# Optimization experiments

Hardware: AMD Instinct MI355X
Metric: run time of the kernel (lower is better)

## Reference

```python
import jax, jax.numpy as jnp
import numpy as np

B, T, C = 1, 2048, 2048
N_HEAD, N_KV = 32, 8
HD = C // N_HEAD            # 64
N_REP = N_HEAD // N_KV      # 4
WINDOW = 512                # sliding_window
N_GLOBAL = 16               # n_global_tokens


def setup_inputs() -> dict:
    key = jax.random.key(0)
    ks = jax.random.split(key, 5)
    x = jax.random.normal(ks[0], (B, T, C), jnp.float32)
    # standard RoPE frequency tables, shape (T, HD//2)
    inv_freq = 1.0 / (10000.0 ** (np.arange(0, HD, 2, dtype=np.float32) / HD))
    ang = np.outer(np.arange(T, dtype=np.float32), inv_freq)
    freqs_cos = jnp.asarray(np.cos(ang), jnp.float32)
    freqs_sin = jnp.asarray(np.sin(ang), jnp.float32)
    s = 0.02
    wq = jax.random.normal(ks[1], (C, C), jnp.float32) * s
    wk = jax.random.normal(ks[2], (N_KV * HD, C), jnp.float32) * s
    wv = jax.random.normal(ks[3], (N_KV * HD, C), jnp.float32) * s
    wo = jax.random.normal(ks[4], (C, C), jnp.float32) * s
    return {"x": x, "freqs_cos": freqs_cos, "freqs_sin": freqs_sin,
            "wq": wq, "wk": wk, "wv": wv, "wo": wo}


def _apply_rope(xh, fc, fs):
    # xh: (B, H, T, HD); fc/fs: (T, HD//2) broadcast over (B, H)
    xr = xh.reshape(*xh.shape[:-1], HD // 2, 2)
    x0, x1 = xr[..., 0], xr[..., 1]
    fc = fc[None, None]
    fs = fs[None, None]
    out = jnp.stack([x0 * fc - x1 * fs, x0 * fs + x1 * fc], axis=-1)
    return out.reshape(xh.shape)


def reference(x, freqs_cos, freqs_sin, wq, wk, wv, wo):
    Bx, Tx, Cx = x.shape
    q = (x @ wq.T).reshape(Bx, Tx, N_HEAD, HD).transpose(0, 2, 1, 3)   # (B,Hq,T,hd)
    k = (x @ wk.T).reshape(Bx, Tx, N_KV, HD).transpose(0, 2, 1, 3)     # (B,Hkv,T,hd)
    v = (x @ wv.T).reshape(Bx, Tx, N_KV, HD).transpose(0, 2, 1, 3)
    q = _apply_rope(q, freqs_cos, freqs_sin)
    k = _apply_rope(k, freqs_cos, freqs_sin)

    # GQA: group query heads over shared kv heads instead of repeat_kv
    qg = q.reshape(Bx, N_KV, N_REP, Tx, HD)
    scale = 1.0 / float(np.sqrt(HD))
    scores = jnp.einsum('bgrqd,bgkd->bgrqk', qg, k) * scale  # (B,G,R,T,T)

    # sliding-window causal mask with global tokens (kv_cache=None branch)
    q_pos = jnp.arange(Tx)[:, None]
    k_pos = jnp.arange(Tx)[None, :]
    mask = (k_pos <= q_pos) & (k_pos >= q_pos - (WINDOW - 1))
    mask = mask | (k_pos < N_GLOBAL)
    # note: global columns combined with causal rows always leave >=1 valid key
    scores = jnp.where(mask[None, None, None], scores, -jnp.inf)
    probs = jax.nn.softmax(scores, axis=-1)

    y = jnp.einsum('bgrqk,bgkd->bgrqd', probs, v)
    y = y.reshape(Bx, N_HEAD, Tx, HD).transpose(0, 2, 1, 3).reshape(Bx, Tx, Cx)
    return y @ wo.T  # dropout p=0 in eval
```

## Files before the change

kernel.cpp:

```cpp
#include <hip/hip_runtime.h>
#include <hip/hip_bf16.h>

using short8 = __attribute__((ext_vector_type(8))) short;
using f32x4  = __attribute__((ext_vector_type(4))) float;
using f32x16 = __attribute__((ext_vector_type(16))) float;
using int4v  = __attribute__((ext_vector_type(4))) int;

#define T_SEQ  2048
#define C_DIM  2048
#define NH     32
#define NKV    8
#define HD     64
#define WINDOW 512
#define NGLOB  16

__device__ inline ushort f2bf(float f) {
  union { float f; unsigned u; } v; v.f = f;
  unsigned u = v.u;
  u += 0x7fffu + ((u >> 16) & 1u);
  return (ushort)(u >> 16);
}
__device__ inline float bf2f(ushort h) {
  union { unsigned u; float f; } v; v.u = ((unsigned)h) << 16;
  return v.f;
}

__device__ __forceinline__ void gl_lds16(const ushort* g, ushort* l) {
  __builtin_amdgcn_global_load_lds(
      (const __attribute__((address_space(1))) void*)g,
      (__attribute__((address_space(3))) void*)l, 16, 0, 0);
}

__device__ __forceinline__ f32x16 zero16() {
  f32x16 v;
#pragma unroll
  for (int i = 0; i < 16; i++) v[i] = 0.f;
  return v;
}

__global__ void cvt_f32_bf16(const float* __restrict__ in, ushort* __restrict__ out, int n8) {
  int i = blockIdx.x * blockDim.x + threadIdx.x;
  int stride = gridDim.x * blockDim.x;
  for (; i < n8; i += stride) {
    f32x4 a = *reinterpret_cast<const f32x4*>(in + (size_t)i * 8);
    f32x4 b = *reinterpret_cast<const f32x4*>(in + (size_t)i * 8 + 4);
    short8 o;
#pragma unroll
    for (int j = 0; j < 4; j++) { o[j] = (short)f2bf(a[j]); o[4 + j] = (short)f2bf(b[j]); }
    *reinterpret_cast<short8*>(out + (size_t)i * 8) = o;
  }
}

template <int MODE>
__global__ __launch_bounds__(512) void gemm2p(const ushort* __restrict__ A,
                                              const ushort* __restrict__ B0,
                                              const ushort* __restrict__ B1,
                                              const ushort* __restrict__ B2,
                                              void* __restrict__ C0,
                                              void* __restrict__ C1,
                                              void* __restrict__ C2,
                                              int K) {
  __shared__ ushort As[2][2][128][32];
  __shared__ ushort Bs[2][2][128][32];
  const int tid  = threadIdx.x;
  const int lane = tid & 63;
  const int wid  = tid >> 6;
  const int wr = wid >> 2, wc = wid & 3;
  const int r16 = lane & 15, g16 = (lane >> 4) & 3;
  const int bx = blockIdx.x, by = blockIdx.y;

  const ushort* Brow;
  void* Cout;
  int ldc, col0;
  if constexpr (MODE == 1) {
    if (bx < 16)      { Brow = B0 + (size_t)bx * 128 * K;        Cout = C0; ldc = 2048; col0 = bx * 128; }
    else if (bx < 20) { Brow = B1 + (size_t)(bx - 16) * 128 * K; Cout = C1; ldc = 512;  col0 = (bx - 16) * 128; }
    else              { Brow = B2 + (size_t)(bx - 20) * 128 * K; Cout = C2; ldc = 512;  col0 = (bx - 20) * 128; }
  } else {
    Brow = B0 + (size_t)bx * 128 * K; Cout = C0; ldc = 2048; col0 = bx * 128;
  }
  const ushort* Arow = A + (size_t)by * 128 * K;

  f32x4 acc[4][2];
#pragma unroll
  for (int i = 0; i < 4; i++)
#pragma unroll
    for (int j = 0; j < 2; j++) acc[i][j] = (f32x4){0.f, 0.f, 0.f, 0.f};

  const int srow = tid >> 2, scch = tid & 3;
  const int ssc  = scch ^ ((srow >> 1) & 3);
  const size_t agoff = (size_t)srow * K + ssc * 8;
  const int rchunk = (g16 ^ ((r16 >> 1) & 3)) * 8;

  const int nt = K >> 6;
  int d = 0;

#define STAGE(dd, k0)                                                         \
  {                                                                           \
    _Pragma("unroll") for (int kk = 0; kk < 2; kk++) {                        \
      gl_lds16(&Arow[agoff + (k0) + kk * 32], &As[dd][kk][srow][scch * 8]);   \
      gl_lds16(&Brow[agoff + (k0) + kk * 32], &Bs[dd][kk][srow][scch * 8]);   \
    }                                                                         \
  }

  STAGE(0, 0);
  __syncthreads();

  for (int t = 0; t < nt; ++t) {
    if (t + 1 < nt) STAGE(d ^ 1, (t + 1) * 64);
#pragma unroll
    for (int kk = 0; kk < 2; kk++) {
      short8 af[4], bfv[2];
#pragma unroll
      for (int i = 0; i < 4; i++)
        af[i] = *reinterpret_cast<const short8*>(&As[d][kk][wr * 64 + i * 16 + r16][rchunk]);
#pragma unroll
      for (int j = 0; j < 2; j++)
        bfv[j] = *reinterpret_cast<const short8*>(&Bs[d][kk][wc * 32 + j * 16 + r16][rchunk]);
#pragma unroll
      for (int i = 0; i < 4; i++)
#pragma unroll
        for (int j = 0; j < 2; j++)
          acc[i][j] = __builtin_amdgcn_mfma_f32_16x16x32_bf16(af[i], bfv[j], acc[i][j], 0, 0, 0);
    }
    __syncthreads();
    d ^= 1;
  }
#undef STAGE

#pragma unroll
  for (int i = 0; i < 4; i++)
#pragma unroll
    for (int j = 0; j < 2; j++) {
      int col = col0 + wc * 32 + j * 16 + r16;
#pragma unroll
      for (int r = 0; r < 4; r++) {
        int row = by * 128 + wr * 64 + i * 16 + g16 * 4 + r;
        if constexpr (MODE == 0) ((float*)Cout)[(size_t)row * ldc + col] = acc[i][j][r];
        else                     ((ushort*)Cout)[(size_t)row * ldc + col] = f2bf(acc[i][j][r]);
      }
    }
}

__global__ void rope2(ushort* __restrict__ Qb, ushort* __restrict__ Kb,
                      const float* __restrict__ fc, const float* __restrict__ fs) {
  int idx = blockIdx.x * blockDim.x + threadIdx.x;
  const int QN = T_SEQ * NH * 8;
  ushort* X; int t, hh, c, ld;
  if (idx < QN) { X = Qb; c = idx & 7; hh = (idx >> 3) & 31; t = idx >> 8; ld = NH * HD; }
  else { idx -= QN; X = Kb; c = idx & 7; hh = (idx >> 3) & 7; t = idx >> 6; ld = NKV * HD; }
  size_t base = (size_t)t * ld + hh * HD + c * 8;
  short8 v = *reinterpret_cast<const short8*>(&X[base]);
  f32x4 cc = *reinterpret_cast<const f32x4*>(&fc[t * 32 + c * 4]);
  f32x4 ss = *reinterpret_cast<const f32x4*>(&fs[t * 32 + c * 4]);
  short8 o;
#pragma unroll
  for (int j = 0; j < 4; j++) {
    float x0 = bf2f((ushort)v[2 * j]), x1 = bf2f((ushort)v[2 * j + 1]);
    o[2 * j]     = (short)f2bf(x0 * cc[j] - x1 * ss[j]);
    o[2 * j + 1] = (short)f2bf(x0 * ss[j] + x1 * cc[j]);
  }
  *reinterpret_cast<short8*>(&X[base]) = o;
}

__global__ __launch_bounds__(256) void transpose_bf16(const ushort* __restrict__ in,
                                                      ushort* __restrict__ out,
                                                      int R, int Cc) {
  __shared__ ushort tile[64][72];
  int tr = blockIdx.y * 64, tc = blockIdx.x * 64;
  int tid = threadIdx.x;
#pragma unroll
  for (int s = 0; s < 2; s++) {
    int idx = tid + s * 256;
    int row = idx >> 3, c8 = idx & 7;
    short8 v = *reinterpret_cast<const short8*>(&in[(size_t)(tr + row) * Cc + tc + c8 * 8]);
#pragma unroll
    for (int j = 0; j < 8; j++) tile[row][c8 * 8 + j] = (ushort)v[j];
  }
  __syncthreads();
#pragma unroll
  for (int s = 0; s < 2; s++) {
    int idx = tid + s * 256;
    int orow = idx >> 3, c8 = idx & 7;
    short8 v;
#pragma unroll
    for (int j = 0; j < 8; j++) v[j] = (short)tile[c8 * 8 + j][orow];
    *reinterpret_cast<short8*>(&out[(size_t)(tc + orow) * R + tr + c8 * 8]) = v;
  }
}

__global__ __launch_bounds__(256) void attn32(const ushort* __restrict__ Q,
                                              const ushort* __restrict__ K,
                                              const ushort* __restrict__ Vt,
                                              ushort* __restrict__ Y) {
  __shared__ ushort Ot[4][32][72];
  const int lane = threadIdx.x & 63;
  const int wv   = threadIdx.x >> 6;
  const int h  = blockIdx.x >> 4;
  const int qt = ((blockIdx.x & 15) << 2) + wv;
  const int q0 = qt << 5;
  const int g  = h >> 2;
  const int l31 = lane & 31, hi = lane >> 5;
  const int hi8 = hi << 3, hi4 = hi << 2;
  const int qrow = q0 + l31;
  const float KLOG = 0.125f * 1.44269504089f;

  short8 qf[4];
#pragma unroll
  for (int s = 0; s < 4; s++)
    qf[s] = *reinterpret_cast<const short8*>(&Q[(size_t)qrow * C_DIM + h * HD + s * 16 + hi8]);

  f32x16 o[2] = { zero16(), zero16() };
  float mrow = -1e30f, ssum = 0.f;

  auto pack8 = [&](const float* pp) -> short8 {
    unsigned wA, wB, wC, wD;
    asm("v_cvt_pk_bf16_f32 %0, %1, %2" : "=v"(wA) : "v"(pp[0]), "v"(pp[1]));
    asm("v_cvt_pk_bf16_f32 %0, %1, %2" : "=v"(wB) : "v"(pp[2]), "v"(pp[3]));
    asm("v_cvt_pk_bf16_f32 %0, %1, %2" : "=v"(wC) : "v"(pp[4]), "v"(pp[5]));
    asm("v_cvt_pk_bf16_f32 %0, %1, %2" : "=v"(wD) : "v"(pp[6]), "v"(pp[7]));
    asm("v_permlane32_swap_b32 %0, %1" : "+v"(wA), "+v"(wC));
    asm("v_permlane32_swap_b32 %0, %1" : "+v"(wB), "+v"(wD));
    int4v w4 = { (int)wA, (int)wB, (int)wC, (int)wD };
    return __builtin_bit_cast(short8, w4);
  };

  auto tile = [&](int kb, bool domask) {
    f32x16 sa = zero16();
#pragma unroll
    for (int s = 0; s < 4; s++) {
      short8 kf = *reinterpret_cast<const short8*>(
          &K[(size_t)(kb + l31) * (NKV * HD) + g * HD + s * 16 + hi8]);
      sa = __builtin_amdgcn_mfma_f32_32x32x16_bf16(kf, qf[s], sa, 0, 0, 0);
    }
    float p[16];
#pragma unroll
    for (int r = 0; r < 16; r++) p[r] = sa[r] * KLOG;
    if (domask) {
#pragma unroll
      for (int r = 0; r < 16; r++) {
        int kidx = kb + (r & 3) + 8 * (r >> 2) + hi4;
        bool ok = ((kidx <= qrow) && (kidx >= qrow - (WINDOW - 1))) || (kidx < NGLOB);
        p[r] = ok ? p[r] : -1e30f;
      }
    }
    float t[16];
#pragma unroll
    for (int r = 0; r < 16; r++) t[r] = p[r];
#pragma unroll
    for (int st = 1; st < 16; st <<= 1)
#pragma unroll
      for (int i = 0; i < 16; i += 2 * st) t[i] = fmaxf(t[i], t[i + st]);
    float pmax = fmaxf(t[0], __shfl_xor(t[0], 32));
    if (!__all(pmax <= mrow + 8.0f)) {
      float mnew = fmaxf(mrow, pmax);
      float corr = exp2f(mrow - mnew);
      ssum *= corr;
#pragma unroll
      for (int r = 0; r < 16; r++) { o[0][r] *= corr; o[1][r] *= corr; }
      mrow = mnew;
    }
#pragma unroll
    for (int r = 0; r < 16; r++) p[r] = exp2f(p[r] - mrow);
    float su[16];
#pragma unroll
    for (int r = 0; r < 16; r++) su[r] = p[r];
#pragma unroll
    for (int st = 1; st < 16; st <<= 1)
#pragma unroll
      for (int i = 0; i < 16; i += 2 * st) su[i] += su[i + st];
    ssum += su[0];
    short8 pb0 = pack8(&p[0]);
    short8 pb1 = pack8(&p[8]);
#pragma unroll
    for (int ntl = 0; ntl < 2; ntl++) {
      const ushort* vp = &Vt[(size_t)(g * HD + ntl * 32 + l31) * T_SEQ + kb + hi8];
      short8 v0 = *reinterpret_cast<const short8*>(vp);
      short8 v1 = *reinterpret_cast<const short8*>(vp + 16);
      o[ntl] = __builtin_amdgcn_mfma_f32_32x32x16_bf16(v0, pb0, o[ntl], 0, 0, 0);
      o[ntl] = __builtin_amdgcn_mfma_f32_32x32x16_bf16(v1, pb1, o[ntl], 0, 0, 0);
    }
  };

  tile(0, true);
  int wsr = (q0 - (WINDOW - 1)) >> 5;
  int wstart = (wsr < 1) ? 32 : (wsr << 5);
  for (int kb = wstart; kb <= q0; kb += 32)
    tile(kb, (kb < q0 - 480) || (kb == q0));

  float stot = ssum + __shfl_xor(ssum, 32);
  float inv = 1.0f / stot;

#pragma unroll
  for (int ntl = 0; ntl < 2; ntl++)
#pragma unroll
    for (int r = 0; r < 16; r++) {
      int dim = ntl * 32 + (r & 3) + 8 * (r >> 2) + hi4;
      Ot[wv][l31][dim] = f2bf(o[ntl][r] * inv);
    }
  __syncthreads();
  int qq = lane >> 1, hf = lane & 1;
#pragma unroll
  for (int c = 0; c < 4; c++) {
    short8 vv = *reinterpret_cast<const short8*>(&Ot[wv][qq][hf * 32 + c * 8]);
    *reinterpret_cast<short8*>(&Y[(size_t)(q0 + qq) * C_DIM + h * HD + hf * 32 + c * 8]) = vv;
  }
}

extern "C" void kernel_launch(void* const* d_in, const int* in_sizes, int n_in,
                              void* d_out, int out_size, void* d_ws, size_t ws_size,
                              hipStream_t stream) {
  const float* x  = (const float*)d_in[0];
  const float* fc = (const float*)d_in[1];
  const float* fs = (const float*)d_in[2];
  const float* wq = (const float*)d_in[3];
  const float* wk = (const float*)d_in[4];
  const float* wv = (const float*)d_in[5];
  const float* wo = (const float*)d_in[6];
  float* out = (float*)d_out;

  const size_t SZ_X = (size_t)T_SEQ * C_DIM;
  const size_t SZ_W = (size_t)(NKV * HD) * C_DIM;

  ushort* xb  = (ushort*)d_ws;
  ushort* wqb = xb  + SZ_X;
  ushort* wkb = wqb + SZ_X;
  ushort* wvb = wkb + SZ_W;
  ushort* wob = wvb + SZ_W;
  ushort* Qb  = wob + SZ_X;
  ushort* Kb  = Qb  + SZ_X;
  ushort* Vb  = Kb  + SZ_W;
  ushort* Vt  = Vb  + SZ_W;
  ushort* Yb  = Vt  + SZ_W;

  cvt_f32_bf16<<<512, 256, 0, stream>>>(x,  xb,  (int)(SZ_X / 8));
  cvt_f32_bf16<<<512, 256, 0, stream>>>(wq, wqb, (int)(SZ_X / 8));
  cvt_f32_bf16<<<256, 256, 0, stream>>>(wk, wkb, (int)(SZ_W / 8));
  cvt_f32_bf16<<<256, 256, 0, stream>>>(wv, wvb, (int)(SZ_W / 8));
  cvt_f32_bf16<<<512, 256, 0, stream>>>(wo, wob, (int)(SZ_X / 8));

  gemm2p<1><<<dim3(24, 16), 512, 0, stream>>>(xb, wqb, wkb, wvb, Qb, Kb, Vb, C_DIM);

  rope2<<<(T_SEQ * (NH + NKV) * 8) / 256, 256, 0, stream>>>(Qb, Kb, fc, fs);
  transpose_bf16<<<dim3((NKV * HD) / 64, T_SEQ / 64), 256, 0, stream>>>(Vb, Vt, T_SEQ, NKV * HD);

  attn32<<<512, 256, 0, stream>>>(Qb, Kb, Vt, Yb);

  gemm2p<0><<<dim3(16, 16), 512, 0, stream>>>(Yb, wob, nullptr, nullptr, out, nullptr, nullptr, C_DIM);
}
```

Before: 142.4 us.

## Fuse conversion launches, fold softmax scale into RoPE, double-buffer attention KV loads

The five f32-to-bf16 conversion launches become one fused kernel with a flat index space. The softmax scale times log2(e) is now applied to Q during RoPE, which removes a per-score multiply in attention. The attention grid is remapped so the four waves of a block handle the four query heads of one KV group on the same query tile, so they share K/V rows in cache. The KV tile loop is software-pipelined with two register buffers, and MFMA sections are raised with s_setprio. Costs are extra register pressure from the prefetch buffers and an additional bf16 rounding of the pre-scaled Q.

```diff
diff --git a/kernel.cpp b/kernel.cpp
--- a/kernel.cpp
+++ b/kernel.cpp
@@ -38,16 +38,29 @@
   return v;
 }
 
-__global__ void cvt_f32_bf16(const float* __restrict__ in, ushort* __restrict__ out, int n8) {
-  int i = blockIdx.x * blockDim.x + threadIdx.x;
+__global__ void cvt_all(const float* __restrict__ s0, ushort* __restrict__ d0, int n0,
+                        const float* __restrict__ s1, ushort* __restrict__ d1, int n1,
+                        const float* __restrict__ s2, ushort* __restrict__ d2, int n2,
+                        const float* __restrict__ s3, ushort* __restrict__ d3, int n3,
+                        const float* __restrict__ s4, ushort* __restrict__ d4, int n4) {
+  int total = n0 + n1 + n2 + n3 + n4;
   int stride = gridDim.x * blockDim.x;
-  for (; i < n8; i += stride) {
-    f32x4 a = *reinterpret_cast<const f32x4*>(in + (size_t)i * 8);
-    f32x4 b = *reinterpret_cast<const f32x4*>(in + (size_t)i * 8 + 4);
+  for (int i = blockIdx.x * blockDim.x + threadIdx.x; i < total; i += stride) {
+    int j = i; const float* s; ushort* d;
+    if (j < n0) { s = s0; d = d0; }
+    else { j -= n0;
+      if (j < n1) { s = s1; d = d1; }
+      else { j -= n1;
+        if (j < n2) { s = s2; d = d2; }
+        else { j -= n2;
+          if (j < n3) { s = s3; d = d3; }
+          else { j -= n3; s = s4; d = d4; } } } }
+    f32x4 a = *reinterpret_cast<const f32x4*>(s + (size_t)j * 8);
+    f32x4 b = *reinterpret_cast<const f32x4*>(s + (size_t)j * 8 + 4);
     short8 o;
 #pragma unroll
-    for (int j = 0; j < 4; j++) { o[j] = (short)f2bf(a[j]); o[4 + j] = (short)f2bf(b[j]); }
-    *reinterpret_cast<short8*>(out + (size_t)i * 8) = o;
+    for (int k = 0; k < 4; k++) { o[k] = (short)f2bf(a[k]); o[4 + k] = (short)f2bf(b[k]); }
+    *reinterpret_cast<short8*>(d + (size_t)j * 8) = o;
   }
 }
 
@@ -146,9 +159,11 @@
                       const float* __restrict__ fc, const float* __restrict__ fs) {
   int idx = blockIdx.x * blockDim.x + threadIdx.x;
   const int QN = T_SEQ * NH * 8;
-  ushort* X; int t, hh, c, ld;
-  if (idx < QN) { X = Qb; c = idx & 7; hh = (idx >> 3) & 31; t = idx >> 8; ld = NH * HD; }
-  else { idx -= QN; X = Kb; c = idx & 7; hh = (idx >> 3) & 7; t = idx >> 6; ld = NKV * HD; }
+  ushort* X; int t, hh, c, ld; float ksc;
+  if (idx < QN) { X = Qb; c = idx & 7; hh = (idx >> 3) & 31; t = idx >> 8; ld = NH * HD;
+                  ksc = 0.125f * 1.44269504089f; }
+  else { idx -= QN; X = Kb; c = idx & 7; hh = (idx >> 3) & 7; t = idx >> 6; ld = NKV * HD;
+         ksc = 1.0f; }
   size_t base = (size_t)t * ld + hh * HD + c * 8;
   short8 v = *reinterpret_cast<const short8*>(&X[base]);
   f32x4 cc = *reinterpret_cast<const f32x4*>(&fc[t * 32 + c * 4]);
@@ -157,8 +172,8 @@
 #pragma unroll
   for (int j = 0; j < 4; j++) {
     float x0 = bf2f((ushort)v[2 * j]), x1 = bf2f((ushort)v[2 * j + 1]);
-    o[2 * j]     = (short)f2bf(x0 * cc[j] - x1 * ss[j]);
-    o[2 * j + 1] = (short)f2bf(x0 * ss[j] + x1 * cc[j]);
+    o[2 * j]     = (short)f2bf((x0 * cc[j] - x1 * ss[j]) * ksc);
+    o[2 * j + 1] = (short)f2bf((x0 * ss[j] + x1 * cc[j]) * ksc);
   }
   *reinterpret_cast<short8*>(&X[base]) = o;
 }
@@ -196,14 +211,13 @@
   __shared__ ushort Ot[4][32][72];
   const int lane = threadIdx.x & 63;
   const int wv   = threadIdx.x >> 6;
-  const int h  = blockIdx.x >> 4;
-  const int qt = ((blockIdx.x & 15) << 2) + wv;
+  const int g  = blockIdx.x >> 6;
+  const int qt = blockIdx.x & 63;
+  const int h  = g * 4 + wv;
   const int q0 = qt << 5;
-  const int g  = h >> 2;
   const int l31 = lane & 31, hi = lane >> 5;
   const int hi8 = hi << 3, hi4 = hi << 2;
   const int qrow = q0 + l31;
-  const float KLOG = 0.125f * 1.44269504089f;
 
   short8 qf[4];
 #pragma unroll
@@ -225,68 +239,86 @@
     return __builtin_bit_cast(short8, w4);
   };
 
-  auto tile = [&](int kb, bool domask) {
-    f32x16 sa = zero16();
-#pragma unroll
-    for (int s = 0; s < 4; s++) {
-      short8 kf = *reinterpret_cast<const short8*>(
-          &K[(size_t)(kb + l31) * (NKV * HD) + g * HD + s * 16 + hi8]);
-      sa = __builtin_amdgcn_mfma_f32_32x32x16_bf16(kf, qf[s], sa, 0, 0, 0);
-    }
-    float p[16];
-#pragma unroll
-    for (int r = 0; r < 16; r++) p[r] = sa[r] * KLOG;
-    if (domask) {
-#pragma unroll
-      for (int r = 0; r < 16; r++) {
-        int kidx = kb + (r & 3) + 8 * (r >> 2) + hi4;
-        bool ok = ((kidx <= qrow) && (kidx >= qrow - (WINDOW - 1))) || (kidx < NGLOB);
-        p[r] = ok ? p[r] : -1e30f;
-      }
-    }
-    float t[16];
-#pragma unroll
-    for (int r = 0; r < 16; r++) t[r] = p[r];
-#pragma unroll
-    for (int st = 1; st < 16; st <<= 1)
-#pragma unroll
-      for (int i = 0; i < 16; i += 2 * st) t[i] = fmaxf(t[i], t[i + st]);
-    float pmax = fmaxf(t[0], __shfl_xor(t[0], 32));
-    if (!__all(pmax <= mrow + 8.0f)) {
-      float mnew = fmaxf(mrow, pmax);
-      float corr = exp2f(mrow - mnew);
-      ssum *= corr;
-#pragma unroll
-      for (int r = 0; r < 16; r++) { o[0][r] *= corr; o[1][r] *= corr; }
-      mrow = mnew;
-    }
-#pragma unroll
-    for (int r = 0; r < 16; r++) p[r] = exp2f(p[r] - mrow);
-    float su[16];
-#pragma unroll
-    for (int r = 0; r < 16; r++) su[r] = p[r];
-#pragma unroll
-    for (int st = 1; st < 16; st <<= 1)
-#pragma unroll
-      for (int i = 0; i < 16; i += 2 * st) su[i] += su[i + st];
-    ssum += su[0];
-    short8 pb0 = pack8(&p[0]);
-    short8 pb1 = pack8(&p[8]);
-#pragma unroll
-    for (int ntl = 0; ntl < 2; ntl++) {
-      const ushort* vp = &Vt[(size_t)(g * HD + ntl * 32 + l31) * T_SEQ + kb + hi8];
-      short8 v0 = *reinterpret_cast<const short8*>(vp);
-      short8 v1 = *reinterpret_cast<const short8*>(vp + 16);
-      o[ntl] = __builtin_amdgcn_mfma_f32_32x32x16_bf16(v0, pb0, o[ntl], 0, 0, 0);
-      o[ntl] = __builtin_amdgcn_mfma_f32_32x32x16_bf16(v1, pb1, o[ntl], 0, 0, 0);
-    }
-  };
-
-  tile(0, true);
+#define LOADKV(kreg, vreg, kb)                                                     \
+  {                                                                                \
+    _Pragma("unroll") for (int s = 0; s < 4; s++)                                  \
+      kreg[s] = *reinterpret_cast<const short8*>(                                  \
+          &K[(size_t)((kb) + l31) * (NKV * HD) + g * HD + s * 16 + hi8]);          \
+    _Pragma("unroll") for (int ntl = 0; ntl < 2; ntl++) {                          \
+      const ushort* vp = &Vt[(size_t)(g * HD + ntl * 32 + l31) * T_SEQ + (kb) + hi8]; \
+      vreg[2 * ntl]     = *reinterpret_cast<const short8*>(vp);                    \
+      vreg[2 * ntl + 1] = *reinterpret_cast<const short8*>(vp + 16);               \
+    }                                                                              \
+  }
+
+#define PROCESS(kreg, vreg, kb, domask)                                            \
+  {                                                                                \
+    f32x16 sa = zero16();                                                          \
+    __builtin_amdgcn_s_setprio(1);                                                 \
+    _Pragma("unroll") for (int s = 0; s < 4; s++)                                  \
+      sa = __builtin_amdgcn_mfma_f32_32x32x16_bf16(kreg[s], qf[s], sa, 0, 0, 0);   \
+    __builtin_amdgcn_s_setprio(0);                                                 \
+    float p[16];                                                                   \
+    _Pragma("unroll") for (int r = 0; r < 16; r++) p[r] = sa[r];                   \
+    if (domask) {                                                                  \
+      _Pragma("unroll") for (int r = 0; r < 16; r++) {                             \
+        int kidx = (kb) + (r & 3) + 8 * (r >> 2) + hi4;                            \
+        bool ok = ((kidx <= qrow) && (kidx >= qrow - (WINDOW - 1))) || (kidx < NGLOB); \
+        p[r] = ok ? p[r] : -1e30f;                                                 \
+      }                                                                            \
+    }                                                                              \
+    float t[16];                                                                   \
+    _Pragma("unroll") for (int r = 0; r < 16; r++) t[r] = p[r];                    \
+    _Pragma("unroll") for (int st = 1; st < 16; st <<= 1)                          \
+      _Pragma("unroll") for (int i2 = 0; i2 < 16; i2 += 2 * st)                    \
+        t[i2] = fmaxf(t[i2], t[i2 + st]);                                          \
+    float pmax = fmaxf(t[0], __shfl_xor(t[0], 32));                                \
+    if (!__all(pmax <= mrow + 8.0f)) {                                             \
+      float mnew = fmaxf(mrow, pmax);                                              \
+      float corr = exp2f(mrow - mnew);                                             \
+      ssum *= corr;                                                                \
+      _Pragma("unroll") for (int r = 0; r < 16; r++) { o[0][r] *= corr; o[1][r] *= corr; } \
+      mrow = mnew;                                                                 \
+    }                                                                              \
+    _Pragma("unroll") for (int r = 0; r < 16; r++) p[r] = exp2f(p[r] - mrow);      \
+    float su[16];                                                                  \
+    _Pragma("unroll") for (int r = 0; r < 16; r++) su[r] = p[r];                   \
+    _Pragma("unroll") for (int st = 1; st < 16; st <<= 1)                          \
+      _Pragma("unroll") for (int i2 = 0; i2 < 16; i2 += 2 * st)                    \
+        su[i2] += su[i2 + st];                                                     \
+    ssum += su[0];                                                                 \
+    short8 pb0 = pack8(&p[0]);                                                     \
+    short8 pb1 = pack8(&p[8]);                                                     \
+    __builtin_amdgcn_s_setprio(1);                                                 \
+    o[0] = __builtin_amdgcn_mfma_f32_32x32x16_bf16(vreg[0], pb0, o[0], 0, 0, 0);   \
+    o[0] = __builtin_amdgcn_mfma_f32_32x32x16_bf16(vreg[1], pb1, o[0], 0, 0, 0);   \
+    o[1] = __builtin_amdgcn_mfma_f32_32x32x16_bf16(vreg[2], pb0, o[1], 0, 0, 0);   \
+    o[1] = __builtin_amdgcn_mfma_f32_32x32x16_bf16(vreg[3], pb1, o[1], 0, 0, 0);   \
+    __builtin_amdgcn_s_setprio(0);                                                 \
+  }
+
   int wsr = (q0 - (WINDOW - 1)) >> 5;
   int wstart = (wsr < 1) ? 32 : (wsr << 5);
-  for (int kb = wstart; kb <= q0; kb += 32)
-    tile(kb, (kb < q0 - 480) || (kb == q0));
+  int ntw = (q0 >= wstart) ? (((q0 - wstart) >> 5) + 1) : 0;
+  const int NT = 1 + ntw;
+
+  short8 kA[4], vA[4], kB[4], vB[4];
+  LOADKV(kA, vA, 0);
+
+  for (int i = 0; i < NT; i += 2) {
+    int kb_i = (i == 0) ? 0 : wstart + (i - 1) * 32;
+    if (i + 1 < NT) { int kb1 = wstart + i * 32; LOADKV(kB, vB, kb1); }
+    bool m_i = (i == 0) || (kb_i < q0 - 480) || (kb_i == q0);
+    PROCESS(kA, vA, kb_i, m_i);
+    if (i + 1 < NT) {
+      int kb1 = wstart + i * 32;
+      if (i + 2 < NT) { int kb2 = wstart + (i + 1) * 32; LOADKV(kA, vA, kb2); }
+      bool m1 = (kb1 < q0 - 480) || (kb1 == q0);
+      PROCESS(kB, vB, kb1, m1);
+    }
+  }
+#undef LOADKV
+#undef PROCESS
 
   float stot = ssum + __shfl_xor(ssum, 32);
   float inv = 1.0f / stot;
@@ -333,11 +365,11 @@
   ushort* Vt  = Vb  + SZ_W;
   ushort* Yb  = Vt  + SZ_W;
 
-  cvt_f32_bf16<<<512, 256, 0, stream>>>(x,  xb,  (int)(SZ_X / 8));
-  cvt_f32_bf16<<<512, 256, 0, stream>>>(wq, wqb, (int)(SZ_X / 8));
-  cvt_f32_bf16<<<256, 256, 0, stream>>>(wk, wkb, (int)(SZ_W / 8));
-  cvt_f32_bf16<<<256, 256, 0, stream>>>(wv, wvb, (int)(SZ_W / 8));
-  cvt_f32_bf16<<<512, 256, 0, stream>>>(wo, wob, (int)(SZ_X / 8));
+  cvt_all<<<1024, 256, 0, stream>>>(x,  xb,  (int)(SZ_X / 8),
+                                    wq, wqb, (int)(SZ_X / 8),
+                                    wk, wkb, (int)(SZ_W / 8),
+                                    wv, wvb, (int)(SZ_W / 8),
+                                    wo, wob, (int)(SZ_X / 8));
 
   gemm2p<1><<<dim3(24, 16), 512, 0, stream>>>(xb, wqb, wkb, wvb, Qb, Kb, Vb, C_DIM);
 
```

Measured after the change: 135.2 us. -5.1%, faster.
